# Kernel tuning notes

Measured on AMD Instinct MI355X. Metric: run time of the kernel, lower is better.

Reference implementation:

```python
import jax, jax.numpy as jnp
import numpy as np

B, N, D_IN, H, D_OUT = 64, 512, 1024, 1024, 1024
EPS = 1e-5          # torch BatchNorm1d default eps
NEG_SLOPE = 0.01    # torch leaky_relu default


def setup_inputs() -> dict:
    key = jax.random.key(0)
    ks = jax.random.split(key, 12)
    s_in = 1.0 / np.sqrt(D_IN)
    s_h = 1.0 / np.sqrt(H)
    return {
        "x": jax.random.normal(ks[0], (B, N, D_IN), dtype=jnp.float32),
        # weights stored as [in, out] so y = x @ W + b
        "W1": jax.random.uniform(ks[1], (D_IN, H), jnp.float32, -s_in, s_in),
        "b1": jax.random.uniform(ks[2], (H,), jnp.float32, -s_in, s_in),
        "gamma": jnp.ones((N,), jnp.float32),
        "beta": jnp.zeros((N,), jnp.float32),
        "W2": jax.random.uniform(ks[3], (D_IN, H), jnp.float32, -s_in, s_in),
        "b2": jax.random.uniform(ks[4], (H,), jnp.float32, -s_in, s_in),
        "W3": jax.random.uniform(ks[5], (H, D_OUT), jnp.float32, -s_h, s_h),
        "b3": jax.random.uniform(ks[6], (D_OUT,), jnp.float32, -s_h, s_h),
        "W4": jax.random.uniform(ks[7], (D_IN, D_OUT), jnp.float32, -s_in, s_in),
        "b4": jax.random.uniform(ks[8], (D_OUT,), jnp.float32, -s_in, s_in),
    }


def reference(x, W1, b1, gamma, beta, W2, b2, W3, b3, W4, b4):
    h = W1.shape[1]
    # theta_x = leaky_relu(bn(l1(x)))
    t = x @ W1 + b1                                   # [B, N, H]
    # BatchNorm1d(num_input): channel dim is N; train-mode batch stats over (B, H)
    mean = jnp.mean(t, axis=(0, 2), keepdims=True)
    var = jnp.var(t, axis=(0, 2), keepdims=True)      # biased variance (torch norm path)
    t = gamma[None, :, None] * (t - mean) * jax.lax.rsqrt(var + EPS) + beta[None, :, None]
    t = jnp.where(t >= 0, t, NEG_SLOPE * t)
    # sigma = theta @ M @ theta^T with M = (I - 1/h)/h  ==  mean-center rows then scale by 1/h
    tM = (t - jnp.mean(t, axis=-1, keepdims=True)) / h  # [B, N, H]
    sigma = jnp.einsum("bnh,bmh->bnm", tM, t)           # [B, N, N]
    att = sigma / jnp.sqrt(jnp.float32(h))              # normal_factor = sqrt(hidden)
    # GLOBAL softmax over the full flattened N*N matrix per batch element
    bsz, n = x.shape[0], x.shape[1]
    att = jax.nn.softmax(att.reshape(bsz, -1), axis=1).reshape(bsz, n, n)
    g = x @ W2 + b2                                     # [B, N, H]
    p = jnp.einsum("bnm,bmh->bnh", att, g) @ W3 + b3    # [B, N, D_OUT]
    phi = x @ W4 + b4                                   # [B, N, D_OUT]
    return phi + p
```

## Files before the change

### kernel.cpp

```cpp
#include <hip/hip_runtime.h>
#include <hip/hip_bf16.h>

typedef _Float16 f16x8 __attribute__((ext_vector_type(8)));
typedef _Float16 f16x4 __attribute__((ext_vector_type(4)));
typedef float    f32x4 __attribute__((ext_vector_type(4)));

#define EPS_ 1e-5f

__device__ __forceinline__ void gload_lds16(const _Float16* g, _Float16* l) {
    __builtin_amdgcn_global_load_lds(
        (const __attribute__((address_space(1))) void*)g,
        (__attribute__((address_space(3))) void*)l, 16, 0, 0);
}


__global__ void k_cvt_f16(const float* __restrict__ in, _Float16* __restrict__ out, int n4) {
    int i = blockIdx.x * blockDim.x + threadIdx.x;
    int stride = gridDim.x * blockDim.x;
    const float4* in4 = (const float4*)in;
    for (; i < n4; i += stride) {
        float4 v = in4[i];
        f16x4 o;
        o[0] = (_Float16)v.x; o[1] = (_Float16)v.y;
        o[2] = (_Float16)v.z; o[3] = (_Float16)v.w;
        *(f16x4*)(out + (size_t)i * 4) = o;
    }
}

__global__ void k_transpose_w3(const float* __restrict__ Wa, const float* __restrict__ Wb,
                               const float* __restrict__ Wc, _Float16* __restrict__ oa,
                               _Float16* __restrict__ ob, _Float16* __restrict__ oc) {
    const float* in = blockIdx.z == 0 ? Wa : (blockIdx.z == 1 ? Wb : Wc);
    _Float16* out   = blockIdx.z == 0 ? oa : (blockIdx.z == 1 ? ob : oc);
    __shared__ float tile[32][33];
    int bx = blockIdx.x * 32;
    int by = blockIdx.y * 32;
    int tx = threadIdx.x, ty = threadIdx.y;
    #pragma unroll
    for (int r = 0; r < 32; r += 8)
        tile[ty + r][tx] = in[(size_t)(by + ty + r) * 1024 + bx + tx];
    __syncthreads();
    #pragma unroll
    for (int r = 0; r < 32; r += 8)
        out[(size_t)(bx + ty + r) * 1024 + by + tx] = (_Float16)tile[tx][ty + r];
}

__global__ void k_b23(const float* __restrict__ b2, const float* __restrict__ W3,
                      float* __restrict__ b23) {
    const int oo = threadIdx.x & 63, hc = threadIdx.x >> 6;
    const int o = blockIdx.x * 64 + oo;
    float s = 0.f;
    for (int h = hc * 256; h < hc * 256 + 256; ++h) s += b2[h] * W3[(size_t)h * 1024 + o];
    __shared__ float red[4][64];
    red[hc][oo] = s;
    __syncthreads();
    if (threadIdx.x < 64) {
        int o2 = blockIdx.x * 64 + threadIdx.x;
        b23[o2] = red[0][threadIdx.x] + red[1][threadIdx.x] + red[2][threadIdx.x] + red[3][threadIdx.x];
    }
}


__global__ void k_bnstats2(const float* __restrict__ spart, const float* __restrict__ gamma,
                           const float* __restrict__ beta, float* __restrict__ scale,
                           float* __restrict__ shift) {
    const int n = blockIdx.x, tid = threadIdx.x;
    const int b = tid >> 2, c = tid & 3;
    const int row = b * 512 + n;
    float s = spart[c * 32768 + row];
    float q = spart[131072 + c * 32768 + row];
    #pragma unroll
    for (int o = 32; o > 0; o >>= 1) { s += __shfl_down(s, o); q += __shfl_down(q, o); }
    __shared__ float rs_[4], rq_[4];
    int lane = tid & 63, w = tid >> 6;
    if (lane == 0) { rs_[w] = s; rq_[w] = q; }
    __syncthreads();
    if (tid == 0) {
        float S = rs_[0] + rs_[1] + rs_[2] + rs_[3];
        float Q = rq_[0] + rq_[1] + rq_[2] + rq_[3];
        float mean = S * (1.f / 65536.f);
        float var  = Q * (1.f / 65536.f) - mean * mean;
        float r = rsqrtf(var + EPS_);
        float sc = gamma[n] * r;
        scale[n] = sc;
        shift[n] = beta[n] - mean * sc;
    }
}

__global__ void k_bnorm(const _Float16* __restrict__ t, const float* __restrict__ scale,
                        const float* __restrict__ shift, _Float16* __restrict__ theta,
                        float* __restrict__ mu) {
    const int row = blockIdx.x, tid = threadIdx.x;
    const int n = row & 511;
    const float sc = scale[n], sh = shift[n];
    f16x4 v = *(const f16x4*)(t + (size_t)row * 1024 + tid * 4);
    float a0 = fmaf((float)v[0], sc, sh); a0 = a0 >= 0.f ? a0 : 0.01f * a0;
    float a1 = fmaf((float)v[1], sc, sh); a1 = a1 >= 0.f ? a1 : 0.01f * a1;
    float a2 = fmaf((float)v[2], sc, sh); a2 = a2 >= 0.f ? a2 : 0.01f * a2;
    float a3 = fmaf((float)v[3], sc, sh); a3 = a3 >= 0.f ? a3 : 0.01f * a3;
    float s = a0 + a1 + a2 + a3;
    #pragma unroll
    for (int o = 32; o > 0; o >>= 1) s += __shfl_down(s, o);
    __shared__ float red[4];
    int lane = tid & 63, w = tid >> 6;
    if (lane == 0) red[w] = s;
    __syncthreads();
    const float mean = (red[0] + red[1] + red[2] + red[3]) * (1.f / 1024.f);
    f16x4 th;
    th[0] = (_Float16)a0; th[1] = (_Float16)a1; th[2] = (_Float16)a2; th[3] = (_Float16)a3;
    *(f16x4*)(theta + (size_t)row * 1024 + tid * 4) = th;
    if (tid == 0) mu[row] = mean;
}

__global__ void k_ssum(const float* __restrict__ part, float* __restrict__ rsum,
                       float* __restrict__ ssum) {
    const int b = blockIdx.x, j = threadIdx.x;
    const int idx = b * 512 + j;
    float s = part[idx] + part[32768 + idx] + part[65536 + idx] + part[98304 + idx];
    rsum[idx] = s;
    #pragma unroll
    for (int o = 32; o > 0; o >>= 1) s += __shfl_down(s, o);
    __shared__ float red[8];
    if ((j & 63) == 0) red[j >> 6] = s;
    __syncthreads();
    if (j == 0) {
        float tt = 0.f;
        #pragma unroll
        for (int k = 0; k < 8; k++) tt += red[k];
        ssum[b] = tt;
    }
}


template <int MODE>
__global__ __launch_bounds__(256) void k_gemm(
    const _Float16* __restrict__ A0, const _Float16* __restrict__ B0,
    const float* __restrict__ auxA, float* __restrict__ auxW,
    void* __restrict__ outp) {

    constexpr int BK = 32;
    __shared__ _Float16 Al[4096];
    __shared__ _Float16 Bl[4096];

    const int tid = threadIdx.x, lane = tid & 63, w = tid >> 6;
    const int wm = w >> 1, wn = w & 1;

    int bm, bn, bz;
    if constexpr (MODE == 1) {
        const int p = blockIdx.x;
        if (p < 4)      { bm = 0; bn = p; }
        else if (p < 7) { bm = 1; bn = p - 3; }
        else if (p < 9) { bm = 2; bn = p - 5; }
        else            { bm = 3; bn = 3; }
        bz = blockIdx.z;
    } else {
        bm = blockIdx.x; bn = blockIdx.y; bz = blockIdx.z;
    }

    const int srow = tid >> 2;
    const int skofs = ((tid & 3) ^ ((tid >> 3) & 3)) * 8;
    _Float16* lA0 = &Al[(w * 64) * 8];
    _Float16* lA1 = &Al[(256 + w * 64) * 8];
    _Float16* lB0 = &Bl[(w * 64) * 8];
    _Float16* lB1 = &Bl[(256 + w * 64) * 8];

    const int lr = lane & 15, kg = lane >> 4;
    const int kswz = kg ^ ((lr >> 1) & 3);

    f32x4 acc[4][4] = {};

    const size_t aO = ((size_t)bz * 512 + bm * 128) * 1024;
    const size_t bO = ((size_t)bz * 512 + bn * 128) * 1024;
    for (int k0 = 0; k0 < 1024; k0 += BK) {
        gload_lds16(A0 + aO + (size_t)srow * 1024 + k0 + skofs, lA0);
        gload_lds16(A0 + aO + (size_t)(srow + 64) * 1024 + k0 + skofs, lA1);
        gload_lds16(B0 + bO + (size_t)srow * 1024 + k0 + skofs, lB0);
        gload_lds16(B0 + bO + (size_t)(srow + 64) * 1024 + k0 + skofs, lB1);
        __syncthreads();
        f16x8 af[4], bf[4];
        #pragma unroll
        for (int m = 0; m < 4; m++)
            af[m] = *(const f16x8*)&Al[((wm * 64 + m * 16 + lr) * 4 + kswz) * 8];
        #pragma unroll
        for (int n = 0; n < 4; n++)
            bf[n] = *(const f16x8*)&Bl[((wn * 64 + n * 16 + lr) * 4 + kswz) * 8];
        #pragma unroll
        for (int m = 0; m < 4; m++)
            #pragma unroll
            for (int n = 0; n < 4; n++)
                acc[m][n] = __builtin_amdgcn_mfma_f32_16x16x32_f16(af[m], bf[n], acc[m][n], 0, 0, 0);
        __syncthreads();
    }

    if constexpr (MODE == 1) {
        __shared__ float rbuf[2][128];
        __shared__ float cbuf[2][128];
        __shared__ _Float16 T[128][136];
        const bool diag = (bm == bn);
        _Float16* o = (_Float16*)outp + (size_t)bz * 262144;
        float csn[4] = {0.f, 0.f, 0.f, 0.f};
        #pragma unroll
        for (int m = 0; m < 4; m++) {
            const int r0 = wm * 64 + m * 16 + kg * 4;
            float rs[4] = {0.f, 0.f, 0.f, 0.f};
            #pragma unroll
            for (int n = 0; n < 4; n++) {
                const int cl = wn * 64 + n * 16 + lr;
                const int gc = bn * 128 + cl;
                const float mj = auxA[bz * 512 + gc];
                f16x4 pk;
                #pragma unroll
                for (int i = 0; i < 4; i++) {
                    const float mi = auxA[bz * 512 + bm * 128 + r0 + i];
                    const float e = __expf(acc[m][n][i] * (1.f / 32768.f) - mi * mj * (1.f / 32.f));
                    o[(size_t)(bm * 128 + r0 + i) * 512 + gc] = (_Float16)e;
                    pk[i] = (_Float16)e;
                    rs[i] += e;
                    csn[n] += e;
                }
                if (!diag) *(f16x4*)&T[cl][r0] = pk;
            }
            #pragma unroll
            for (int i = 0; i < 4; i++) {
                float v = rs[i];
                v += __shfl_xor(v, 1); v += __shfl_xor(v, 2);
                v += __shfl_xor(v, 4); v += __shfl_xor(v, 8);
                if (lr == 0) rbuf[wn][r0 + i] = v;
            }
        }
        if (!diag) {
            #pragma unroll
            for (int n = 0; n < 4; n++) {
                float v = csn[n];
                v += __shfl_xor(v, 16); v += __shfl_xor(v, 32);
                if (kg == 0) cbuf[wm][wn * 64 + n * 16 + lr] = v;
            }
        }
        __syncthreads();
        if (tid < 128) {
            auxW[(size_t)bn * 32768 + bz * 512 + bm * 128 + tid] = rbuf[0][tid] + rbuf[1][tid];
            if (!diag)
                auxW[(size_t)bm * 32768 + bz * 512 + bn * 128 + tid] = cbuf[0][tid] + cbuf[1][tid];
        }
        if (!diag) {
            #pragma unroll
            for (int k = 0; k < 8; k++) {
                const int q = k * 256 + tid;
                const int c = q >> 4, j = q & 15;
                f16x8 v = *(const f16x8*)&T[c][j * 8];
                *(f16x8*)(o + (size_t)(bn * 128 + c) * 512 + bm * 128 + j * 8) = v;
            }
        }
    } else {
        _Float16* o = (_Float16*)outp;
        #pragma unroll
        for (int m = 0; m < 4; m++) {
            #pragma unroll
            for (int n = 0; n < 4; n++) {
                const int r0 = wm * 64 + m * 16 + kg * 4;
                const int gc = bn * 128 + wn * 64 + n * 16 + lr;
                #pragma unroll
                for (int i = 0; i < 4; i++)
                    o[(size_t)(bm * 128 + r0 + i) * 1024 + gc] = (_Float16)acc[m][n][i];
            }
        }
    }
}


template <int MODE>
__global__ __launch_bounds__(512) void k_gemm8(
    const _Float16* __restrict__ A0, const _Float16* __restrict__ B0,
    const _Float16* __restrict__ A1, const _Float16* __restrict__ B1,
    const float* __restrict__ biasf, const float* __restrict__ biasg,
    const float* __restrict__ auxA, const float* __restrict__ auxB,
    const float* __restrict__ sumptr, void* __restrict__ outp) {

    __shared__ _Float16 LA[32768];
    __shared__ _Float16 LB[32768];

    const int tid = threadIdx.x, lane = tid & 63, wid = tid >> 6;
    const int wm = wid >> 2, wn = wid & 3;
    const int lr = lane & 15, kq = lane >> 4;

    int bm, bn, bz = 0;
    if constexpr (MODE == 6) {
        const int swz = (blockIdx.x & 7) * 128 + (blockIdx.x >> 3);
        bm = swz >> 3; bn = swz & 7;
    } else {
        const int swz = (blockIdx.x & 7) * 64 + (blockIdx.x >> 3);
        if constexpr (MODE == 3) { bz = swz >> 3; bm = (swz >> 2) & 1; bn = swz & 3; }
        else { bm = swz >> 2; bn = swz & 3; }
    }

    constexpr int NITER = (MODE == 3) ? 12 : 8;
    float oscale = 1.f;
    if constexpr (MODE == 3) oscale = 1.f / sumptr[bz];

    const int i0 = tid >> 3;
    const int kgs = (tid & 7) ^ (i0 & 7);

    auto STAGE = [&](int g, int isA, int h) {
        const _Float16* P; int ld; size_t off; int kk;
        if constexpr (MODE == 3) {
            if (g < 8) {
                kk = g * 64;
                if (isA) { P = A0; ld = 512;  off = (size_t)bz * 262144 + (size_t)bm * 256 * 512; }
                else     { P = B0; ld = 512;  off = (size_t)bz * 524288 + (size_t)bn * 256 * 512; }
            } else {
                kk = (g - 8) * 64;
                if (isA) { P = A1; ld = 1024; off = ((size_t)bz * 512 + bm * 256) * 1024; }
                else     { P = B1; ld = 1024; off = (size_t)bn * 256 * 1024; }
            }
        } else {
            kk = g * 64;
            if (isA) { P = A0; ld = 1024; off = (size_t)bm * 256 * 1024; }
            else     { P = B0; ld = 1024; off = (size_t)bn * 256 * 1024; }
        }
        const int l0 = isA ? (h * 64 + i0)
                           : ((i0 >> 5) * 64 + h * 32 + (i0 & 31));
        const int l1 = isA ? (128 + h * 64 + i0)
                           : (((i0 >> 5) + 2) * 64 + h * 32 + (i0 & 31));
        _Float16* dst = (isA ? LA : LB) + ((g & 1) * 2 + h) * 8192 + wid * 512;
        gload_lds16(P + off + (size_t)l0 * ld + kk + kgs * 8, dst);
        gload_lds16(P + off + (size_t)l1 * ld + kk + kgs * 8, dst + 4096);
    };

    f32x4 acc[8][4] = {};

    STAGE(0, 1, 0); STAGE(0, 0, 0); STAGE(0, 0, 1); STAGE(0, 1, 1);
    STAGE(1, 0, 0); STAGE(1, 0, 1); STAGE(1, 1, 0);
    asm volatile("s_waitcnt vmcnt(6)" ::: "memory");
    __builtin_amdgcn_s_barrier();

    for (int i = 0; i < NITER; ++i) {
        if constexpr (MODE == 3) {
            if (i == 4) {
                #pragma unroll
                for (int m = 0; m < 8; m++)
                    #pragma unroll
                    for (int n = 0; n < 4; n++)
                        #pragma unroll
                        for (int v = 0; v < 4; v++) acc[m][n][v] *= oscale;
            }
        }
        const bool more = (i + 1 < NITER);
        #pragma unroll
        for (int kt = 0; kt < 2; ++kt) {
            f16x8 bf[4][2];
            #pragma unroll
            for (int sub = 0; sub < 4; ++sub) {
                const int ph = kt * 4 + sub;
                if (sub == 0) {
                    #pragma unroll
                    for (int n = 0; n < 4; n++) {
                        const _Float16* Bs = LB + (kt * 2 + (n >> 1)) * 8192;
                        #pragma unroll
                        for (int s = 0; s < 2; s++)
                            bf[n][s] = *(const f16x8*)&Bs[(wn * 32 + (n & 1) * 16 + lr) * 64
                                                           + ((((s << 2) | kq) ^ (lr & 7)) << 3)];
                    }
                }
                const _Float16* As = LA + (kt * 2 + (sub >> 1)) * 8192;
                f16x8 af[2][2];
                #pragma unroll
                for (int j = 0; j < 2; j++) {
                    const int m = sub * 2 + j;
                    #pragma unroll
                    for (int s = 0; s < 2; s++)
                        af[j][s] = *(const f16x8*)&As[(wm * 64 + (m & 3) * 16 + lr) * 64
                                                       + ((((s << 2) | kq) ^ (lr & 7)) << 3)];
                }
                {
                    constexpr int gof[8] = {1, 2, 2, 2, 2, 3, 3, 3};
                    constexpr int isa[8] = {1, 0, 0, 1, 1, 0, 0, 1};
                    constexpr int hh [8] = {1, 0, 1, 0, 1, 0, 1, 0};
                    if (ph == 0 || more) STAGE(2 * i + gof[ph], isa[ph], hh[ph]);
                }
                __builtin_amdgcn_s_barrier();
                asm volatile("s_waitcnt lgkmcnt(0)" ::: "memory");
                __builtin_amdgcn_sched_barrier(0);
                __builtin_amdgcn_s_setprio(1);
                #pragma unroll
                for (int j = 0; j < 2; j++)
                    #pragma unroll
                    for (int n = 0; n < 4; n++)
                        #pragma unroll
                        for (int s = 0; s < 2; s++)
                            acc[sub * 2 + j][n] = __builtin_amdgcn_mfma_f32_16x16x32_f16(
                                af[j][s], bf[n][s], acc[sub * 2 + j][n], 0, 0, 0);
                __builtin_amdgcn_s_setprio(0);
                if (ph == 1) { if (more) asm volatile("s_waitcnt vmcnt(10)" ::: "memory");
                               else      asm volatile("s_waitcnt vmcnt(8)"  ::: "memory"); }
                if (ph == 3) { if (more) asm volatile("s_waitcnt vmcnt(8)"  ::: "memory");
                               else      asm volatile("s_waitcnt vmcnt(2)"  ::: "memory"); }
                if (ph == 5) { if (more) asm volatile("s_waitcnt vmcnt(10)" ::: "memory");
                               else      asm volatile("s_waitcnt vmcnt(0)"  ::: "memory"); }
                if (ph == 7) { if (more) asm volatile("s_waitcnt vmcnt(8)"  ::: "memory"); }
                __builtin_amdgcn_s_barrier();
            }
        }
    }

    if constexpr (MODE == 6) {
        if (bn < 4) {
            _Float16* o = (_Float16*)outp;
            float* sbuf = (float*)LA;
            float* qbuf = (float*)LB;
            __syncthreads();
            #pragma unroll
            for (int m = 0; m < 8; m++) {
                float s4[4] = {0.f, 0.f, 0.f, 0.f}, q4[4] = {0.f, 0.f, 0.f, 0.f};
                const int gr0 = bm * 256 + wm * 128 + m * 16 + kq * 4;
                #pragma unroll
                for (int n = 0; n < 4; n++) {
                    const int gc = bn * 256 + wn * 64 + n * 16 + lr;
                    const float bias = biasf[gc];
                    #pragma unroll
                    for (int i = 0; i < 4; i++) {
                        const float e = acc[m][n][i] + bias;
                        o[(size_t)(gr0 + i) * 1024 + gc] = (_Float16)e;
                        s4[i] += e; q4[i] += e * e;
                    }
                }
                #pragma unroll
                for (int i = 0; i < 4; i++) {
                    float s = s4[i], q = q4[i];
                    s += __shfl_xor(s, 1); q += __shfl_xor(q, 1);
                    s += __shfl_xor(s, 2); q += __shfl_xor(q, 2);
                    s += __shfl_xor(s, 4); q += __shfl_xor(q, 4);
                    s += __shfl_xor(s, 8); q += __shfl_xor(q, 8);
                    if (lr == 0) {
                        const int rl = wm * 128 + m * 16 + kq * 4 + i;
                        sbuf[wn * 256 + rl] = s;
                        qbuf[wn * 256 + rl] = q;
                    }
                }
            }
            __syncthreads();
            if (tid < 256) {
                const float s = sbuf[tid] + sbuf[256 + tid] + sbuf[512 + tid] + sbuf[768 + tid];
                const float q = qbuf[tid] + qbuf[256 + tid] + qbuf[512 + tid] + qbuf[768 + tid];
                float* sp = (float*)auxB;
                const int row = bm * 256 + tid;
                sp[bn * 32768 + row] = s;
                sp[131072 + bn * 32768 + row] = q;
            }
        } else {
            _Float16* o = (_Float16*)B1;
            #pragma unroll
            for (int m = 0; m < 8; m++) {
                #pragma unroll
                for (int n = 0; n < 4; n++) {
                    const int gc = bn * 256 + wn * 64 + n * 16 + lr;
                    const int gr0 = bm * 256 + wm * 128 + m * 16 + kq * 4;
                    const int oc = gc - 1024;
                    const int bb = gr0 >> 9, mm = gr0 & 511;
                    f16x4 pk;
                    #pragma unroll
                    for (int i = 0; i < 4; i++) pk[i] = (_Float16)acc[m][n][i];
                    *(f16x4*)(o + ((size_t)bb * 1024 + oc) * 512 + mm) = pk;
                }
            }
        }
    } else {
        #pragma unroll
        for (int m = 0; m < 8; m++) {
            #pragma unroll
            for (int n = 0; n < 4; n++) {
                const int gc = bn * 256 + wn * 64 + n * 16 + lr;
                const int gr0 = bm * 256 + wm * 128 + m * 16 + kq * 4;
                float* o = (float*)outp;
                const float tail = biasf[gc] + biasg[gc];
                const float b23v = auxB[gc];
                #pragma unroll
                for (int i = 0; i < 4; i++) {
                    const int row = gr0 + i;
                    o[((size_t)bz * 512 + row) * 1024 + gc] =
                        acc[m][n][i] + auxA[bz * 512 + row] * oscale * b23v + tail;
                }
            }
        }
    }
}


extern "C" void kernel_launch(void* const* d_in, const int* in_sizes, int n_in,
                              void* d_out, int out_size, void* d_ws, size_t ws_size,
                              hipStream_t stream) {
    (void)in_sizes; (void)n_in; (void)out_size; (void)ws_size;
    const float* x     = (const float*)d_in[0];
    const float* W1    = (const float*)d_in[1];
    const float* b1    = (const float*)d_in[2];
    const float* gamma = (const float*)d_in[3];
    const float* beta  = (const float*)d_in[4];
    const float* W2    = (const float*)d_in[5];
    const float* b2    = (const float*)d_in[6];
    const float* W3    = (const float*)d_in[7];
    const float* b3    = (const float*)d_in[8];
    const float* W4    = (const float*)d_in[9];
    const float* b4    = (const float*)d_in[10];

    char* wsb = (char*)d_ws;
    const size_t MB = 1024 * 1024;
    _Float16* xb    = (_Float16*)(wsb);
    _Float16* Wcat  = (_Float16*)(wsb + 64 * MB);
    _Float16* W1t   = Wcat;
    _Float16* W23t  = Wcat + 1024 * 1024;
    _Float16* W3t   = (_Float16*)(wsb + 68 * MB);
    _Float16* W4t   = (_Float16*)(wsb + 70 * MB);
    _Float16* W2h   = (_Float16*)(wsb + 72 * MB);
    float*    b23   = (float*)(wsb + 74 * MB);
    float*    scl   = (float*)(wsb + 74 * MB + 8192);
    float*    shf   = (float*)(wsb + 74 * MB + 16384);
    float*    ssum  = (float*)(wsb + 74 * MB + 24576);
    float*    mu    = (float*)(wsb + 75 * MB);
    float*    rsum  = (float*)(wsb + 76 * MB);
    float*    rpart = (float*)(wsb + 77 * MB);
    float*    spart = (float*)(wsb + 78 * MB);
    _Float16* t     = (_Float16*)(wsb + 80 * MB);
    _Float16* theta = (_Float16*)(wsb + 144 * MB);
    _Float16* att   = (_Float16*)(wsb + 208 * MB);
    _Float16* gwt   = (_Float16*)(wsb + 240 * MB);

    k_cvt_f16<<<2048, 256, 0, stream>>>(x, xb, 64 * 512 * 1024 / 4);
    k_cvt_f16<<<1024, 256, 0, stream>>>(W2, W2h, 1024 * 1024 / 4);
    dim3 tb(32, 8), tg3(32, 32, 3);
    k_transpose_w3<<<tg3, tb, 0, stream>>>(W1, W3, W4, W1t, W3t, W4t);
    k_gemm<5><<<dim3(8, 8, 1), 256, 0, stream>>>(W3t, W2h, nullptr, nullptr, W23t);
    k_b23<<<16, 256, 0, stream>>>(b2, W3, b23);
    k_gemm8<6><<<1024, 512, 0, stream>>>(xb, Wcat, nullptr, gwt,
        b1, nullptr, nullptr, spart, nullptr, t);
    k_bnstats2<<<512, 256, 0, stream>>>(spart, gamma, beta, scl, shf);
    k_bnorm<<<32768, 256, 0, stream>>>(t, scl, shf, theta, mu);
    k_gemm<1><<<dim3(10, 1, 64), 256, 0, stream>>>(theta, theta, mu, rpart, att);
    k_ssum<<<64, 512, 0, stream>>>(rpart, rsum, ssum);
    k_gemm8<3><<<512, 512, 0, stream>>>(att, gwt, xb, W4t,
        b3, b4, rsum, b23, ssum, d_out);
}
```

Before: 436.8 us.

## Move symmetric theta Gram GEMM onto 256x256 pipelined kernel with 3 tiles per batch

The sigma = theta·thetaᵀ GEMM with its fused exp/row-sum epilogue moves from the 128x128 single-buffered kernel (10 upper-triangle tiles per batch) to the 512-thread pipelined 256x256 kernel, using 3 upper-triangle tiles per batch (192 blocks). Off-diagonal tiles are transposed through the reused LDS staging buffers with an XOR swizzle, and row/column partial sums now come from 2 column tiles, so the partial-sum reduction reads 2 slices instead of 4. This aims to improve data reuse and MFMA pipelining, but leaves fewer blocks (192) to fill the GPU and adds a larger epilogue per block.

```diff
diff --git a/kernel.cpp b/kernel.cpp
--- a/kernel.cpp
+++ b/kernel.cpp
@@ -116,7 +116,7 @@
                        float* __restrict__ ssum) {
     const int b = blockIdx.x, j = threadIdx.x;
     const int idx = b * 512 + j;
-    float s = part[idx] + part[32768 + idx] + part[65536 + idx] + part[98304 + idx];
+    float s = part[idx] + part[32768 + idx];
     rsum[idx] = s;
     #pragma unroll
     for (int o = 32; o > 0; o >>= 1) s += __shfl_down(s, o);
@@ -132,11 +132,9 @@
 }
 
 
-template <int MODE>
-__global__ __launch_bounds__(256) void k_gemm(
+__global__ __launch_bounds__(256) void k_gemm5(
     const _Float16* __restrict__ A0, const _Float16* __restrict__ B0,
-    const float* __restrict__ auxA, float* __restrict__ auxW,
-    void* __restrict__ outp) {
+    _Float16* __restrict__ outp) {
 
     constexpr int BK = 32;
     __shared__ _Float16 Al[4096];
@@ -144,18 +142,7 @@
 
     const int tid = threadIdx.x, lane = tid & 63, w = tid >> 6;
     const int wm = w >> 1, wn = w & 1;
-
-    int bm, bn, bz;
-    if constexpr (MODE == 1) {
-        const int p = blockIdx.x;
-        if (p < 4)      { bm = 0; bn = p; }
-        else if (p < 7) { bm = 1; bn = p - 3; }
-        else if (p < 9) { bm = 2; bn = p - 5; }
-        else            { bm = 3; bn = 3; }
-        bz = blockIdx.z;
-    } else {
-        bm = blockIdx.x; bn = blockIdx.y; bz = blockIdx.z;
-    }
+    const int bm = blockIdx.x, bn = blockIdx.y;
 
     const int srow = tid >> 2;
     const int skofs = ((tid & 3) ^ ((tid >> 3) & 3)) * 8;
@@ -169,8 +156,8 @@
 
     f32x4 acc[4][4] = {};
 
-    const size_t aO = ((size_t)bz * 512 + bm * 128) * 1024;
-    const size_t bO = ((size_t)bz * 512 + bn * 128) * 1024;
+    const size_t aO = (size_t)bm * 128 * 1024;
+    const size_t bO = (size_t)bn * 128 * 1024;
     for (int k0 = 0; k0 < 1024; k0 += BK) {
         gload_lds16(A0 + aO + (size_t)srow * 1024 + k0 + skofs, lA0);
         gload_lds16(A0 + aO + (size_t)(srow + 64) * 1024 + k0 + skofs, lA1);
@@ -192,77 +179,15 @@
         __syncthreads();
     }
 
-    if constexpr (MODE == 1) {
-        __shared__ float rbuf[2][128];
-        __shared__ float cbuf[2][128];
-        __shared__ _Float16 T[128][136];
-        const bool diag = (bm == bn);
-        _Float16* o = (_Float16*)outp + (size_t)bz * 262144;
-        float csn[4] = {0.f, 0.f, 0.f, 0.f};
-        #pragma unroll
-        for (int m = 0; m < 4; m++) {
+    #pragma unroll
+    for (int m = 0; m < 4; m++) {
+        #pragma unroll
+        for (int n = 0; n < 4; n++) {
             const int r0 = wm * 64 + m * 16 + kg * 4;
-            float rs[4] = {0.f, 0.f, 0.f, 0.f};
-            #pragma unroll
-            for (int n = 0; n < 4; n++) {
-                const int cl = wn * 64 + n * 16 + lr;
-                const int gc = bn * 128 + cl;
-                const float mj = auxA[bz * 512 + gc];
-                f16x4 pk;
-                #pragma unroll
-                for (int i = 0; i < 4; i++) {
-                    const float mi = auxA[bz * 512 + bm * 128 + r0 + i];
-                    const float e = __expf(acc[m][n][i] * (1.f / 32768.f) - mi * mj * (1.f / 32.f));
-                    o[(size_t)(bm * 128 + r0 + i) * 512 + gc] = (_Float16)e;
-                    pk[i] = (_Float16)e;
-                    rs[i] += e;
-                    csn[n] += e;
-                }
-                if (!diag) *(f16x4*)&T[cl][r0] = pk;
-            }
-            #pragma unroll
-            for (int i = 0; i < 4; i++) {
-                float v = rs[i];
-                v += __shfl_xor(v, 1); v += __shfl_xor(v, 2);
-                v += __shfl_xor(v, 4); v += __shfl_xor(v, 8);
-                if (lr == 0) rbuf[wn][r0 + i] = v;
-            }
-        }
-        if (!diag) {
-            #pragma unroll
-            for (int n = 0; n < 4; n++) {
-                float v = csn[n];
-                v += __shfl_xor(v, 16); v += __shfl_xor(v, 32);
-                if (kg == 0) cbuf[wm][wn * 64 + n * 16 + lr] = v;
-            }
-        }
-        __syncthreads();
-        if (tid < 128) {
-            auxW[(size_t)bn * 32768 + bz * 512 + bm * 128 + tid] = rbuf[0][tid] + rbuf[1][tid];
-            if (!diag)
-                auxW[(size_t)bm * 32768 + bz * 512 + bn * 128 + tid] = cbuf[0][tid] + cbuf[1][tid];
-        }
-        if (!diag) {
-            #pragma unroll
-            for (int k = 0; k < 8; k++) {
-                const int q = k * 256 + tid;
-                const int c = q >> 4, j = q & 15;
-                f16x8 v = *(const f16x8*)&T[c][j * 8];
-                *(f16x8*)(o + (size_t)(bn * 128 + c) * 512 + bm * 128 + j * 8) = v;
-            }
-        }
-    } else {
-        _Float16* o = (_Float16*)outp;
-        #pragma unroll
-        for (int m = 0; m < 4; m++) {
-            #pragma unroll
-            for (int n = 0; n < 4; n++) {
-                const int r0 = wm * 64 + m * 16 + kg * 4;
-                const int gc = bn * 128 + wn * 64 + n * 16 + lr;
-                #pragma unroll
-                for (int i = 0; i < 4; i++)
-                    o[(size_t)(bm * 128 + r0 + i) * 1024 + gc] = (_Float16)acc[m][n][i];
-            }
+            const int gc = bn * 128 + wn * 64 + n * 16 + lr;
+            #pragma unroll
+            for (int i = 0; i < 4; i++)
+                outp[(size_t)(bm * 128 + r0 + i) * 1024 + gc] = (_Float16)acc[m][n][i];
         }
     }
 }
@@ -283,10 +208,15 @@
     const int wm = wid >> 2, wn = wid & 3;
     const int lr = lane & 15, kq = lane >> 4;
 
-    int bm, bn, bz = 0;
+    int bm = 0, bn = 0, bz = 0, tm = 0, tn = 0;
     if constexpr (MODE == 6) {
         const int swz = (blockIdx.x & 7) * 128 + (blockIdx.x >> 3);
         bm = swz >> 3; bn = swz & 7;
+    } else if constexpr (MODE == 7) {
+        const int swz = (blockIdx.x & 7) * 24 + (blockIdx.x >> 3);
+        bz = swz / 3;
+        const int pair = swz - bz * 3;
+        tm = pair >> 1; tn = (pair + 1) >> 1;
     } else {
         const int swz = (blockIdx.x & 7) * 64 + (blockIdx.x >> 3);
         if constexpr (MODE == 3) { bz = swz >> 3; bm = (swz >> 2) & 1; bn = swz & 3; }
@@ -296,6 +226,14 @@
     constexpr int NITER = (MODE == 3) ? 12 : 8;
     float oscale = 1.f;
     if constexpr (MODE == 3) oscale = 1.f / sumptr[bz];
+
+    size_t aBase = 0, bBase = 0;
+    if constexpr (MODE == 6) {
+        aBase = (size_t)bm * 256 * 1024; bBase = (size_t)bn * 256 * 1024;
+    } else if constexpr (MODE == 7) {
+        aBase = ((size_t)bz * 512 + tm * 256) * 1024;
+        bBase = ((size_t)bz * 512 + tn * 256) * 1024;
+    }
 
     const int i0 = tid >> 3;
     const int kgs = (tid & 7) ^ (i0 & 7);
@@ -314,8 +252,9 @@
             }
         } else {
             kk = g * 64;
-            if (isA) { P = A0; ld = 1024; off = (size_t)bm * 256 * 1024; }
-            else     { P = B0; ld = 1024; off = (size_t)bn * 256 * 1024; }
+            ld = 1024;
+            if (isA) { P = A0; off = aBase; }
+            else     { P = B0; off = bBase; }
         }
         const int l0 = isA ? (h * 64 + i0)
                            : ((i0 >> 5) * 64 + h * 32 + (i0 & 31));
@@ -461,6 +400,72 @@
                     for (int i = 0; i < 4; i++) pk[i] = (_Float16)acc[m][n][i];
                     *(f16x4*)(o + ((size_t)bb * 1024 + oc) * 512 + mm) = pk;
                 }
+            }
+        }
+    } else if constexpr (MODE == 7) {
+        __shared__ float rbuf7[4][256];
+        __shared__ float cbuf7[2][256];
+        const bool diag = (tm == tn);
+        _Float16* o = (_Float16*)outp + (size_t)bz * 262144;
+        float* rpart = (float*)auxB;
+        float csn[4] = {0.f, 0.f, 0.f, 0.f};
+        __syncthreads();
+        #pragma unroll
+        for (int m = 0; m < 8; m++) {
+            const int rloc = wm * 128 + m * 16 + kq * 4;
+            const int sidx = wm * 32 + m * 4 + kq;
+            float rs[4] = {0.f, 0.f, 0.f, 0.f};
+            #pragma unroll
+            for (int n = 0; n < 4; n++) {
+                const int cl = wn * 64 + n * 16 + lr;
+                const float mj = auxA[bz * 512 + tn * 256 + cl];
+                f16x4 pk;
+                #pragma unroll
+                for (int i = 0; i < 4; i++) {
+                    const float mi = auxA[bz * 512 + tm * 256 + rloc + i];
+                    const float e = __expf(acc[m][n][i] * (1.f / 32768.f) - mi * mj * (1.f / 32.f));
+                    o[(size_t)(tm * 256 + rloc + i) * 512 + tn * 256 + cl] = (_Float16)e;
+                    pk[i] = (_Float16)e;
+                    rs[i] += e;
+                    csn[n] += e;
+                }
+                if (!diag) {
+                    _Float16* Trow = (cl < 128) ? &LA[cl * 256] : &LB[(cl - 128) * 256];
+                    *(f16x4*)&Trow[(sidx ^ ((cl & 7) << 1)) * 4] = pk;
+                }
+            }
+            #pragma unroll
+            for (int i = 0; i < 4; i++) {
+                float v = rs[i];
+                v += __shfl_xor(v, 1); v += __shfl_xor(v, 2);
+                v += __shfl_xor(v, 4); v += __shfl_xor(v, 8);
+                if (lr == 0) rbuf7[wn][rloc + i] = v;
+            }
+        }
+        if (!diag) {
+            #pragma unroll
+            for (int n = 0; n < 4; n++) {
+                float v = csn[n];
+                v += __shfl_xor(v, 16); v += __shfl_xor(v, 32);
+                if (kq == 0) cbuf7[wm][wn * 64 + n * 16 + lr] = v;
+            }
+        }
+        __syncthreads();
+        if (tid < 256) {
+            const float s = rbuf7[0][tid] + rbuf7[1][tid] + rbuf7[2][tid] + rbuf7[3][tid];
+            rpart[tn * 32768 + bz * 512 + tm * 256 + tid] = s;
+            if (!diag)
+                rpart[tm * 32768 + bz * 512 + tn * 256 + tid] =
+                    cbuf7[0][tid] + cbuf7[1][tid];
+        }
+        if (!diag) {
+            #pragma unroll
+            for (int k = 0; k < 16; k++) {
+                const int q = k * 512 + tid;
+                const int c = q >> 5, j = q & 31;
+                const _Float16* Trow = (c < 128) ? &LA[c * 256] : &LB[(c - 128) * 256];
+                f16x8 v = *(const f16x8*)&Trow[(((2 * j) ^ ((c & 7) << 1))) * 4];
+                *(f16x8*)(o + (size_t)(tn * 256 + c) * 512 + tm * 256 + j * 8) = v;
             }
         }
     } else {
@@ -527,13 +532,14 @@
     k_cvt_f16<<<1024, 256, 0, stream>>>(W2, W2h, 1024 * 1024 / 4);
     dim3 tb(32, 8), tg3(32, 32, 3);
     k_transpose_w3<<<tg3, tb, 0, stream>>>(W1, W3, W4, W1t, W3t, W4t);
-    k_gemm<5><<<dim3(8, 8, 1), 256, 0, stream>>>(W3t, W2h, nullptr, nullptr, W23t);
+    k_gemm5<<<dim3(8, 8, 1), 256, 0, stream>>>(W3t, W2h, W23t);
     k_b23<<<16, 256, 0, stream>>>(b2, W3, b23);
     k_gemm8<6><<<1024, 512, 0, stream>>>(xb, Wcat, nullptr, gwt,
         b1, nullptr, nullptr, spart, nullptr, t);
     k_bnstats2<<<512, 256, 0, stream>>>(spart, gamma, beta, scl, shf);
     k_bnorm<<<32768, 256, 0, stream>>>(t, scl, shf, theta, mu);
-    k_gemm<1><<<dim3(10, 1, 64), 256, 0, stream>>>(theta, theta, mu, rpart, att);
+    k_gemm8<7><<<192, 512, 0, stream>>>(theta, theta, nullptr, nullptr,
+        nullptr, nullptr, mu, rpart, nullptr, att);
     k_ssum<<<64, 512, 0, stream>>>(rpart, rsum, ssum);
     k_gemm8<3><<<512, 512, 0, stream>>>(att, gwt, xb, W4t,
         b3, b4, rsum, b23, ssum, d_out);
```

Result: faster. 418.7 us (-4.2%).
